# Kernel tuning notes

Hardware: AMD Instinct MI355X
Metric: run time of the kernel (lower is better)

The kernel has to match this reference:

```python
import jax, jax.numpy as jnp
import numpy as np

B, N, D = 2, 8192, 32
RADIUS2 = 0.03 ** 2
SIM_THRESH = 0.7
MIN_LEAF = 10
EPS = 1e-8


def setup_inputs() -> dict:
    key = jax.random.key(0)
    ks = jax.random.split(key, 5)
    # points scaled to [0, 0.4)^3 so the 0.03 radius finds a few neighbors per point
    points = jax.random.uniform(ks[0], (B, N, 3), dtype=jnp.float32) * 0.4
    embeddings = jax.random.normal(ks[1], (B, N, D), dtype=jnp.float32)
    leaf_mask = jax.random.randint(ks[2], (B, N), 0, 2).astype(jnp.int32)
    # consistency_net: Linear(2D -> D), ReLU, Linear(D -> D); stored as (in, out)
    W1 = jax.random.normal(ks[3], (2 * D, D), dtype=jnp.float32) / np.sqrt(2 * D)
    b1 = jnp.zeros((D,), dtype=jnp.float32)
    W2 = jax.random.normal(ks[4], (D, D), dtype=jnp.float32) / np.sqrt(D)
    b2 = jnp.zeros((D,), dtype=jnp.float32)
    return {"points": points, "embeddings": embeddings, "leaf_mask": leaf_mask,
            "W1": W1, "b1": b1, "W2": W2, "b2": b2}


def reference(points, embeddings, leaf_mask, W1, b1, W2, b2):
    leaf = leaf_mask > 0  # [B,N]
    # squared pairwise distances via ||a||^2 + ||b||^2 - 2 a.b (avoids [B,N,N,3])
    sq = jnp.sum(points * points, axis=-1)  # [B,N]
    d2 = sq[:, :, None] + sq[:, None, :] - 2.0 * jnp.einsum('bnc,bmc->bnm', points, points)
    nb = (d2 < RADIUS2) & leaf[:, None, :]  # neighbor j must be a leaf point
    nb_count = jnp.sum(nb, axis=-1)  # includes self when leaf[i]
    # cosine similarity with per-vector norm clamp (torch F.cosine_similarity eps)
    norms = jnp.maximum(jnp.linalg.norm(embeddings, axis=-1, keepdims=True), EPS)
    en = embeddings / norms
    sim = jnp.einsum('bnd,bmd->bnm', en, en)
    similar = nb & (sim > SIM_THRESH)
    cnt = jnp.sum(similar, axis=-1)  # [B,N]
    w = similar.astype(embeddings.dtype)
    mean_sim = jnp.einsum('bnm,bmd->bnd', w, embeddings) / jnp.maximum(cnt, 1)[..., None]
    combined = jnp.concatenate([embeddings, mean_sim], axis=-1)  # [B,N,2D]
    h = jax.nn.relu(combined @ W1 + b1)
    out = h @ W2 + b2
    batch_ok = (jnp.sum(leaf, axis=-1) >= MIN_LEAF)[:, None]  # skip batches with <10 leaves
    cond = leaf & (nb_count > 1) & (cnt > 0) & batch_ok
    return jnp.where(cond[..., None], out, embeddings)
```

## Files before the change

### kernel.cpp

```cpp
#include <hip/hip_runtime.h>

#define NPTS 8192
#define BN   16384
#define D    32
#define R2   0.0009f
#define SIMT 0.7f
#define RAD  0.03f
#define BLOCK 256
#define PBLOCK 1024
#define PWAVES 16
#define NGRP   (BN / 64)
#define ZBINS 512
#define ZSCALE 1280.0f
#define AFIELDS 34
#define CHUNK 512

#define GLOBAL_AS __attribute__((address_space(1)))
#define LDS_AS    __attribute__((address_space(3)))

__device__ __forceinline__ void g2lds16(const void* g, void* l) {
  __builtin_amdgcn_global_load_lds((const GLOBAL_AS void*)g, (LDS_AS void*)l,
                                   16, 0, 0);
}

__global__ __launch_bounds__(BLOCK) void prep_kernel(
    const float* __restrict__ pts, const float* __restrict__ emb,
    const int* __restrict__ leaf,
    int* __restrict__ histA, int* __restrict__ histL,
    unsigned* __restrict__ done,
    int* __restrict__ rsA, int* __restrict__ rsL,
    int* __restrict__ curA, int* __restrict__ curL,
    float4* __restrict__ sortedA, int* __restrict__ permA,
    float4* __restrict__ pts4L, float* __restrict__ invL,
    float* __restrict__ embL) {
  const int p = blockIdx.x * BLOCK + threadIdx.x;
  const float x = pts[3 * p + 0];
  const float y = pts[3 * p + 1];
  const float z = pts[3 * p + 2];
  const float sq = x * x + y * y + z * z;
  int bin = (int)(z * ZSCALE); if (bin > ZBINS - 1) bin = ZBINS - 1;
  const int b = p >> 13;
  const int lf = leaf[p] > 0;
  atomicAdd(&histA[b * ZBINS + bin], 1);
  if (lf) atomicAdd(&histL[b * ZBINS + bin], 1);

  float4 er[D / 4];
  float ss = 0.f;
  {
    const float4* __restrict__ e4 = (const float4*)(emb + (size_t)p * D);
#pragma unroll
    for (int i = 0; i < D / 4; ++i) {
      er[i] = e4[i];
      ss += er[i].x * er[i].x + er[i].y * er[i].y +
            er[i].z * er[i].z + er[i].w * er[i].w;
    }
  }
  const float inv = 1.0f / fmaxf(sqrtf(ss), 1e-8f);

  __shared__ int islast;
  __syncthreads();
  if (threadIdx.x == 0) {
    const unsigned t = __hip_atomic_fetch_add(&done[0], 1u, __ATOMIC_RELAXED,
                                              __HIP_MEMORY_SCOPE_AGENT);
    islast = (t == gridDim.x - 1);
  }
  __syncthreads();

  if (islast) {
    const int wv = threadIdx.x >> 6;
    const int lane = threadIdx.x & 63;
    const int sb = wv & 1;
    const int* __restrict__ h = (wv < 2) ? histA : histL;
    int* __restrict__ rs = (wv < 2) ? rsA : rsL;
    int* __restrict__ cu = (wv < 2) ? curA : curL;
    int carry = 0;
    for (int c = 0; c < ZBINS / 64; ++c) {
      const int idx = c * 64 + lane;
      const int v = __hip_atomic_load(&h[sb * ZBINS + idx], __ATOMIC_RELAXED,
                                      __HIP_MEMORY_SCOPE_AGENT);
      int incl = v;
#pragma unroll
      for (int off = 1; off < 64; off <<= 1) {
        const int t = __shfl_up(incl, off);
        if (lane >= off) incl += t;
      }
      const int excl = carry + incl - v;
      rs[sb * (ZBINS + 1) + idx] = excl;
      cu[sb * ZBINS + idx] = excl;
      carry += __shfl(incl, 63);
    }
    if (lane == 0) rs[sb * (ZBINS + 1) + ZBINS] = carry;
    __threadfence();
    __syncthreads();
    if (threadIdx.x == 0)
      __hip_atomic_store(&done[1], 1u, __ATOMIC_RELEASE,
                         __HIP_MEMORY_SCOPE_AGENT);
  } else {
    if (threadIdx.x == 0) {
      while (__hip_atomic_load(&done[1], __ATOMIC_ACQUIRE,
                               __HIP_MEMORY_SCOPE_AGENT) == 0)
        __builtin_amdgcn_s_sleep(8);
    }
    __syncthreads();
  }

  const int dst = b * NPTS + atomicAdd(&curA[b * ZBINS + bin], 1);
  sortedA[dst] = make_float4(x, y, z, lf ? inv : -inv);
  permA[dst] = p;

  if (lf) {
    const int dl = b * NPTS + atomicAdd(&curL[b * ZBINS + bin], 1);
    pts4L[dl] = make_float4(x, y, z, 0.5f * (sq - R2));
    invL[dl] = inv;
    float4* __restrict__ d4 = (float4*)(embL + (size_t)dl * D);
#pragma unroll
    for (int k = 0; k < D / 4; ++k) d4[k] = er[k];
  }
}

__global__ __launch_bounds__(PBLOCK) void pair_kernel(
    const float4* __restrict__ sortedA, const int* __restrict__ permA,
    const float4* __restrict__ pts4L, const float* __restrict__ invL,
    const float* __restrict__ embL, const float* __restrict__ emb,
    const int* __restrict__ rsL,
    const float* __restrict__ W1, const float* __restrict__ b1,
    const float* __restrict__ W2, const float* __restrict__ b2,
    float* __restrict__ out) {
  const int ig   = blockIdx.x;
  const int b    = ig >> 7;
  const int lane = threadIdx.x & 63;
  const int wv   = threadIdx.x >> 6;
  const int sg   = ig * 64 + lane;

  __shared__ __align__(16) float4 ptsS[2][CHUNK];
  __shared__ __align__(16) float4 eiS4[64 * 8];
  __shared__ float invIS[64];
  __shared__ int   queueS[PWAVES][128];
  __shared__ float red[AFIELDS][64];
  __shared__ float hS[D][64];
  for (int t = threadIdx.x; t < AFIELDS * 64; t += PBLOCK)
    (&red[0][0])[t] = 0.f;

  const float4 A = sortedA[sg];
  const float inv_i = fabsf(A.w);
  const float mhsq = -0.5f * (A.x * A.x + A.y * A.y + A.z * A.z);
  const int p = permA[sg];

  if (wv == 0) {
    const float4* __restrict__ e4 = (const float4*)(emb + (size_t)p * D);
#pragma unroll
    for (int k = 0; k < D / 4; ++k) eiS4[lane * 8 + (k ^ (lane & 7))] = e4[k];
    invIS[lane] = inv_i;
  }

  float zmin = A.z, zmax = A.z;
#pragma unroll
  for (int off = 1; off < 64; off <<= 1) {
    zmin = fminf(zmin, __shfl_xor(zmin, off));
    zmax = fmaxf(zmax, __shfl_xor(zmax, off));
  }
  int klo = (int)((zmin - RAD) * ZSCALE) - 1; if (klo < 0) klo = 0;
  int khi = (int)((zmax + RAD) * ZSCALE) + 1; if (khi > ZBINS - 1) khi = ZBINS - 1;
  klo = __builtin_amdgcn_readfirstlane(klo);
  khi = __builtin_amdgcn_readfirstlane(khi);
  const int jlo = b * NPTS + rsL[b * (ZBINS + 1) + klo];
  const int jhi = b * NPTS + rsL[b * (ZBINS + 1) + khi + 1];
  const int len = jhi - jlo;

  float nbc = 0.f;
  int qtail = 0, qdone = 0;

  const float4* __restrict__ embQ = (const float4*)embL;

  auto drain = [&](int n) {
    if (lane < n) {
      const int e  = queueS[wv][(qdone + lane) & 127];
      const int il = e & 63;
      const int j  = e >> 6;
      float4 bv[D / 4];
#pragma unroll
      for (int k = 0; k < D / 4; ++k) bv[k] = embQ[(size_t)j * 8 + k];
      const float invj = invL[j];
      float s0 = 0.f, s1 = 0.f, s2 = 0.f, s3 = 0.f;
#pragma unroll
      for (int k = 0; k < D / 4; ++k) {
        const float4 av = eiS4[il * 8 + (k ^ (il & 7))];
        s0 = fmaf(av.x, bv[k].x, s0);
        s1 = fmaf(av.y, bv[k].y, s1);
        s2 = fmaf(av.z, bv[k].z, s2);
        s3 = fmaf(av.w, bv[k].w, s3);
      }
      const float sim = ((s0 + s1) + (s2 + s3)) * invIS[il] * invj;
      if (sim > SIMT) {
        atomicAdd(&red[1][il], 1.0f);
#pragma unroll
        for (int k = 0; k < D / 4; ++k) {
          atomicAdd(&red[2 + 4 * k + 0][il], bv[k].x);
          atomicAdd(&red[2 + 4 * k + 1][il], bv[k].y);
          atomicAdd(&red[2 + 4 * k + 2][il], bv[k].z);
          atomicAdd(&red[2 + 4 * k + 3][il], bv[k].w);
        }
      }
    }
    qdone += n;
  };

  auto stage = [&](int buf, int base, int L) {
    for (int t0 = wv * 64; t0 < L; t0 += PWAVES * 64)
      g2lds16((const char*)pts4L + (((size_t)(base + t0 + lane)) << 4),
              &ptsS[buf][t0]);
  };

  auto process = [&](int buf, int jbase, int L) {
    const int s0 = (L * wv) / PWAVES;
    const int s1 = (L * (wv + 1)) / PWAVES;
    if (s0 >= s1) return;
    float4 c = ptsS[buf][s0];
    for (int jl = s0; jl < s1; ++jl) {
      const float4 cn = ptsS[buf][(jl + 1 < s1) ? (jl + 1) : s0];
      const float t = fmaf(A.z, c.z, fmaf(A.y, c.y, fmaf(A.x, c.x, mhsq)));
      const bool hit = t > c.w;
      const unsigned long long m = __ballot(hit);
      if (m) {
        if (hit) {
          nbc += 1.0f;
          const int below = __popcll(m & ((1ull << lane) - 1ull));
          queueS[wv][(qtail + below) & 127] = ((jbase + jl) << 6) | lane;
        }
        qtail += (int)__popcll(m);
        if (qtail - qdone >= 64) drain(64);
      }
      c = cn;
    }
  };

  const int nch = (len + CHUNK - 1) / CHUNK;
  if (nch > 0) stage(0, jlo, (len < CHUNK) ? len : CHUNK);
  __syncthreads();
  for (int k = 0; k < nch; ++k) {
    const int cur = k & 1;
    if (k + 1 < nch) {
      const int base = jlo + (k + 1) * CHUNK;
      const int L = (jhi - base < CHUNK) ? (jhi - base) : CHUNK;
      stage(cur ^ 1, base, L);
    }
    const int base = jlo + k * CHUNK;
    const int Lc = (jhi - base < CHUNK) ? (jhi - base) : CHUNK;
    process(cur, base, Lc);
    __syncthreads();
  }
  drain(qtail - qdone);

  if (nbc != 0.f) atomicAdd(&red[0][lane], nbc);
  __syncthreads();

  const int kk0 = wv * 8;
  if (wv < 4) {
    const float tcnt = red[1][lane];
    const float rinv = 1.0f / fmaxf(tcnt, 1.0f);
    float h[8];
#pragma unroll
    for (int k = 0; k < 8; ++k) h[k] = b1[kk0 + k];
#pragma unroll
    for (int d = 0; d < D; ++d) {
      const float4 v = eiS4[lane * 8 + ((d >> 2) ^ (lane & 7))];
      const float c = ((d & 3) == 0) ? v.x : ((d & 3) == 1) ? v.y
                    : ((d & 3) == 2) ? v.z : v.w;
      const float* __restrict__ w = W1 + (size_t)d * D + kk0;
#pragma unroll
      for (int k = 0; k < 8; ++k) h[k] = fmaf(c, w[k], h[k]);
    }
#pragma unroll
    for (int d = 0; d < D; ++d) {
      const float c = red[2 + d][lane] * rinv;
      const float* __restrict__ w = W1 + (size_t)(D + d) * D + kk0;
#pragma unroll
      for (int k = 0; k < 8; ++k) h[k] = fmaf(c, w[k], h[k]);
    }
#pragma unroll
    for (int k = 0; k < 8; ++k) hS[kk0 + k][lane] = fmaxf(h[k], 0.f);
  }
  __syncthreads();

  if (wv < 4) {
    float o[8];
#pragma unroll
    for (int m = 0; m < 8; ++m) o[m] = b2[kk0 + m];
#pragma unroll
    for (int k = 0; k < D; ++k) {
      const float hv = hS[k][lane];
      const float* __restrict__ w = W2 + (size_t)k * D + kk0;
#pragma unroll
      for (int m = 0; m < 8; ++m) o[m] = fmaf(hv, w[m], o[m]);
    }
    const float tnbc = red[0][lane];
    const float tcnt = red[1][lane];
    const bool lf = A.w > 0.f;
    const int nleaf = rsL[b * (ZBINS + 1) + ZBINS];
    const bool cond = lf && (tnbc >= 2.0f) && (tcnt >= 1.0f) && (nleaf >= 10);

    float4* outr = (float4*)(out + (size_t)p * D + kk0);
#pragma unroll
    for (int i = 0; i < 2; ++i) {
      float4 v;
      if (cond) { v.x = o[4*i+0]; v.y = o[4*i+1]; v.z = o[4*i+2]; v.w = o[4*i+3]; }
      else      { v = eiS4[lane * 8 + (((kk0 >> 2) + i) ^ (lane & 7))]; }
      outr[i] = v;
    }
  }
}

extern "C" void kernel_launch(void* const* d_in, const int* in_sizes, int n_in,
                              void* d_out, int out_size, void* d_ws, size_t ws_size,
                              hipStream_t stream) {
  (void)in_sizes; (void)n_in; (void)out_size; (void)ws_size;
  const float* pts  = (const float*)d_in[0];
  const float* emb  = (const float*)d_in[1];
  const int*   leaf = (const int*)d_in[2];
  const float* W1   = (const float*)d_in[3];
  const float* b1   = (const float*)d_in[4];
  const float* W2   = (const float*)d_in[5];
  const float* b2   = (const float*)d_in[6];
  float* out = (float*)d_out;

  char* ws = (char*)d_ws;
  size_t off = 0;
  auto alloc = [&](size_t bytes) { void* r = ws + off; off = (off + bytes + 15) & ~(size_t)15; return r; };

  float4*   sortedA = (float4*)alloc((size_t)BN * 16);
  int*      permA   = (int*)alloc((size_t)BN * 4);
  float4*   pts4L   = (float4*)alloc((size_t)(BN + CHUNK) * 16);
  float*    invL    = (float*)alloc((size_t)(BN + CHUNK) * 4);
  float*    embL    = (float*)alloc((size_t)(BN + CHUNK) * D * 4);
  int*      rsA     = (int*)alloc(2 * (ZBINS + 1) * 4);
  int*      rsL     = (int*)alloc(2 * (ZBINS + 1) * 4);
  int*      curA    = (int*)alloc(2 * ZBINS * 4);
  int*      curL    = (int*)alloc(2 * ZBINS * 4);
  int*      histA   = (int*)alloc(2 * ZBINS * 4);
  int*      histL   = (int*)alloc(2 * ZBINS * 4);
  unsigned* done    = (unsigned*)alloc(16);

  hipMemsetAsync(histA, 0, 2 * (2 * ZBINS * 4) + 16, stream);
  prep_kernel<<<BN / BLOCK, BLOCK, 0, stream>>>(
      pts, emb, leaf, histA, histL, done, rsA, rsL, curA, curL,
      sortedA, permA, pts4L, invL, embL);
  pair_kernel<<<NGRP, PBLOCK, 0, stream>>>(
      sortedA, permA, pts4L, invL, embL, emb, rsL,
      W1, b1, W2, b2, out);
}
```

Measured before the change: 107.5 us.

## Split neighbor scan across two blocks per group with last-block reduction

Each 64-point group's candidate j-range is now split in half across two 512-thread blocks instead of one 1024-thread block. Each block writes its partial LDS accumulators to a global slot and bumps a per-group counter, and the last block to arrive sums both partials and runs the MLP epilogue. This is meant to improve load balance and scheduling granularity across CUs when neighbor ranges vary. In exchange it adds a global round-trip, an extra counter memset, and relies on relaxed atomics without an explicit fence to order the partial-sum visibility.

Result: slower. 124.5 us (+15.8%).

```diff
diff --git a/kernel.cpp b/kernel.cpp
--- a/kernel.cpp
+++ b/kernel.cpp
@@ -7,8 +7,9 @@
 #define SIMT 0.7f
 #define RAD  0.03f
 #define BLOCK 256
-#define PBLOCK 1024
-#define PWAVES 16
+#define PBLOCK 512
+#define PWAVES 8
+#define JSPLIT 2
 #define NGRP   (BN / 64)
 #define ZBINS 512
 #define ZSCALE 1280.0f
@@ -125,8 +126,11 @@
     const int* __restrict__ rsL,
     const float* __restrict__ W1, const float* __restrict__ b1,
     const float* __restrict__ W2, const float* __restrict__ b2,
+    float* __restrict__ accG, int* __restrict__ pairdone,
     float* __restrict__ out) {
-  const int ig   = blockIdx.x;
+  const int bid  = blockIdx.x;
+  const int ig   = bid >> 1;
+  const int js   = bid & 1;
   const int b    = ig >> 7;
   const int lane = threadIdx.x & 63;
   const int wv   = threadIdx.x >> 6;
@@ -138,6 +142,7 @@
   __shared__ int   queueS[PWAVES][128];
   __shared__ float red[AFIELDS][64];
   __shared__ float hS[D][64];
+  __shared__ int   islast;
   for (int t = threadIdx.x; t < AFIELDS * 64; t += PBLOCK)
     (&red[0][0])[t] = 0.f;
 
@@ -166,6 +171,11 @@
   const int jlo = b * NPTS + rsL[b * (ZBINS + 1) + klo];
   const int jhi = b * NPTS + rsL[b * (ZBINS + 1) + khi + 1];
   const int len = jhi - jlo;
+  int blo = jlo + (len * js) / JSPLIT;
+  int bhi = jlo + (len * (js + 1)) / JSPLIT;
+  blo = __builtin_amdgcn_readfirstlane(blo);
+  bhi = __builtin_amdgcn_readfirstlane(bhi);
+  const int blen = bhi - blo;
 
   float nbc = 0.f;
   int qtail = 0, qdone = 0;
@@ -234,24 +244,53 @@
     }
   };
 
-  const int nch = (len + CHUNK - 1) / CHUNK;
-  if (nch > 0) stage(0, jlo, (len < CHUNK) ? len : CHUNK);
+  const int nch = (blen + CHUNK - 1) / CHUNK;
+  if (nch > 0) stage(0, blo, (blen < CHUNK) ? blen : CHUNK);
   __syncthreads();
   for (int k = 0; k < nch; ++k) {
     const int cur = k & 1;
     if (k + 1 < nch) {
-      const int base = jlo + (k + 1) * CHUNK;
-      const int L = (jhi - base < CHUNK) ? (jhi - base) : CHUNK;
+      const int base = blo + (k + 1) * CHUNK;
+      const int L = (bhi - base < CHUNK) ? (bhi - base) : CHUNK;
       stage(cur ^ 1, base, L);
     }
-    const int base = jlo + k * CHUNK;
-    const int Lc = (jhi - base < CHUNK) ? (jhi - base) : CHUNK;
+    const int base = blo + k * CHUNK;
+    const int Lc = (bhi - base < CHUNK) ? (bhi - base) : CHUNK;
     process(cur, base, Lc);
     __syncthreads();
   }
   drain(qtail - qdone);
 
   if (nbc != 0.f) atomicAdd(&red[0][lane], nbc);
+  __syncthreads();
+
+  {
+    float* __restrict__ slot = accG + (size_t)bid * (AFIELDS * 64);
+    const float* __restrict__ rf = &red[0][0];
+    for (int t = threadIdx.x; t < AFIELDS * 64; t += PBLOCK)
+      __hip_atomic_store(&slot[t], rf[t], __ATOMIC_RELAXED,
+                         __HIP_MEMORY_SCOPE_AGENT);
+  }
+  __syncthreads();
+  if (threadIdx.x == 0) {
+    const unsigned t = __hip_atomic_fetch_add(
+        (unsigned*)&pairdone[ig], 1u, __ATOMIC_RELAXED,
+        __HIP_MEMORY_SCOPE_AGENT);
+    islast = (t == JSPLIT - 1);
+  }
+  __syncthreads();
+  if (!islast) return;
+
+  {
+    const float* __restrict__ s0 = accG + (size_t)(ig * 2 + 0) * (AFIELDS * 64);
+    const float* __restrict__ s1 = accG + (size_t)(ig * 2 + 1) * (AFIELDS * 64);
+    float* __restrict__ rf = &red[0][0];
+    for (int t = threadIdx.x; t < AFIELDS * 64; t += PBLOCK)
+      rf[t] = __hip_atomic_load(&s0[t], __ATOMIC_RELAXED,
+                                __HIP_MEMORY_SCOPE_AGENT) +
+              __hip_atomic_load(&s1[t], __ATOMIC_RELAXED,
+                                __HIP_MEMORY_SCOPE_AGENT);
+  }
   __syncthreads();
 
   const int kk0 = wv * 8;
@@ -332,6 +371,7 @@
   float4*   pts4L   = (float4*)alloc((size_t)(BN + CHUNK) * 16);
   float*    invL    = (float*)alloc((size_t)(BN + CHUNK) * 4);
   float*    embL    = (float*)alloc((size_t)(BN + CHUNK) * D * 4);
+  float*    accG    = (float*)alloc((size_t)NGRP * JSPLIT * AFIELDS * 64 * 4);
   int*      rsA     = (int*)alloc(2 * (ZBINS + 1) * 4);
   int*      rsL     = (int*)alloc(2 * (ZBINS + 1) * 4);
   int*      curA    = (int*)alloc(2 * ZBINS * 4);
@@ -339,12 +379,13 @@
   int*      histA   = (int*)alloc(2 * ZBINS * 4);
   int*      histL   = (int*)alloc(2 * ZBINS * 4);
   unsigned* done    = (unsigned*)alloc(16);
-
-  hipMemsetAsync(histA, 0, 2 * (2 * ZBINS * 4) + 16, stream);
+  int*      pairdone= (int*)alloc(NGRP * 4);
+
+  hipMemsetAsync(histA, 0, 2 * (2 * ZBINS * 4) + 16 + NGRP * 4, stream);
   prep_kernel<<<BN / BLOCK, BLOCK, 0, stream>>>(
       pts, emb, leaf, histA, histL, done, rsA, rsL, curA, curL,
       sortedA, permA, pts4L, invL, embL);
-  pair_kernel<<<NGRP, PBLOCK, 0, stream>>>(
+  pair_kernel<<<NGRP * JSPLIT, PBLOCK, 0, stream>>>(
       sortedA, permA, pts4L, invL, embL, emb, rsL,
-      W1, b1, W2, b2, out);
+      W1, b1, W2, b2, accG, pairdone, out);
 }
```
